# Kernel tuning notes

Hardware: AMD Instinct MI355X
Metric: run time of the kernel (lower is better)

Reference implementation:

```python
import jax, jax.numpy as jnp
import numpy as np

N = 12000   # num_node
D = 128     # hiddenSize
HID = 256   # hidden_channels
B = 512     # batch
L = 20      # citing history length
F = 400     # title_vec + journal_vec
FF = 512    # transformer dim_feedforward
NH = 4      # heads
STDV = float(1.0 / np.sqrt(D))


def _unif(k, shape):
    return jax.random.uniform(k, shape, jnp.float32, -STDV, STDV)


def setup_inputs():
    key = jax.random.key(0)
    ks = jax.random.split(key, 40)
    inp = {}
    inp['embedding'] = _unif(ks[0], (N, D))
    inp['f1_w'] = _unif(ks[1], (D, F)); inp['f1_b'] = _unif(ks[2], (D,))
    # two GNN modules, each a 2-layer GCN (assumed structure)
    inp['gcn0_w1'] = _unif(ks[3], (D, HID)); inp['gcn0_b1'] = _unif(ks[4], (HID,))
    inp['gcn0_w2'] = _unif(ks[5], (HID, D)); inp['gcn0_b2'] = _unif(ks[6], (D,))
    inp['gcn1_w1'] = _unif(ks[7], (D, HID)); inp['gcn1_b1'] = _unif(ks[8], (HID,))
    inp['gcn1_w2'] = _unif(ks[9], (HID, D)); inp['gcn1_b2'] = _unif(ks[10], (D,))
    # transformer encoder layer (post-norm, relu), reset_parameters makes ALL weights uniform
    inp['in_proj_w'] = _unif(ks[11], (3 * D, D)); inp['in_proj_b'] = _unif(ks[12], (3 * D,))
    inp['out_proj_w'] = _unif(ks[13], (D, D)); inp['out_proj_b'] = _unif(ks[14], (D,))
    inp['ln1_s'] = _unif(ks[15], (D,)); inp['ln1_b'] = _unif(ks[16], (D,))
    inp['ff1_w'] = _unif(ks[17], (FF, D)); inp['ff1_b'] = _unif(ks[18], (FF,))
    inp['ff2_w'] = _unif(ks[19], (D, FF)); inp['ff2_b'] = _unif(ks[20], (D,))
    inp['ln2_s'] = _unif(ks[21], (D,)); inp['ln2_b'] = _unif(ks[22], (D,))
    # forward inputs
    inp['adj_mat'] = jax.random.uniform(ks[23], (N, N), jnp.float32) * (2.0 / N)  # ~row-stochastic
    inp['node_feature'] = jax.random.normal(ks[24], (N, F), jnp.float32)
    inp['H_content'] = jax.random.normal(ks[25], (B, 10), jnp.float32)  # unused in forward
    inp['citing'] = jax.random.randint(ks[26], (B,), 0, N)
    inp['h_items'] = jax.random.randint(ks[27], (B,), 0, N)  # unused in forward
    inp['u_seqs'] = jax.random.randint(ks[28], (B, L), 0, N)
    inp['u_seqs_num'] = jax.random.randint(ks[29], (B,), 1, L)  # unused in forward
    return inp


def _layer_norm(x, s, b):
    m = x.mean(-1, keepdims=True)
    v = ((x - m) ** 2).mean(-1, keepdims=True)
    return (x - m) * jax.lax.rsqrt(v + 1e-5) * s + b


def reference(embedding, f1_w, f1_b,
              gcn0_w1, gcn0_b1, gcn0_w2, gcn0_b2,
              gcn1_w1, gcn1_b1, gcn1_w2, gcn1_b2,
              in_proj_w, in_proj_b, out_proj_w, out_proj_b,
              ln1_s, ln1_b, ff1_w, ff1_b, ff2_w, ff2_b, ln2_s, ln2_b,
              adj_mat, node_feature, H_content,
              citing, h_items, u_seqs, u_seqs_num):
    # embedding gate
    nf = node_feature @ f1_w.T + f1_b          # [N, D]
    x = embedding * nf                          # [N, D]
    # GCN stack: each GNN = relu((A x) W1 + b1) -> (A h) W2 + b2
    for (w1, b1, w2, b2) in ((gcn0_w1, gcn0_b1, gcn0_w2, gcn0_b2),
                             (gcn1_w1, gcn1_b1, gcn1_w2, gcn1_b2)):
        h = jax.nn.relu((adj_mat @ x) @ w1 + b1)
        x = (adj_mat @ h) @ w2 + b2
    item = x                                    # [N, D]
    seq = item[u_seqs]                          # [B, L, D]
    # torch TransformerEncoderLayer with batch_first=False: dim0 (B) is the
    # sequence axis, dim1 (L) is the batch axis (faithful to original code).
    qkv = seq @ in_proj_w.T + in_proj_b         # [B, L, 3D]
    q, k, v = jnp.split(qkv, 3, axis=-1)
    dh = D // NH
    q = q.reshape(B, L, NH, dh) * (1.0 / np.sqrt(dh))
    k = k.reshape(B, L, NH, dh)
    v = v.reshape(B, L, NH, dh)
    att = jax.nn.softmax(jnp.einsum('snhd,tnhd->nhst', q, k), axis=-1)  # attn over seq axis s,t=B
    o = jnp.einsum('nhst,tnhd->snhd', att, v).reshape(B, L, D)
    o = o @ out_proj_w.T + out_proj_b
    x1 = _layer_norm(seq + o, ln1_s, ln1_b)
    ff = jax.nn.relu(x1 @ ff1_w.T + ff1_b) @ ff2_w.T + ff2_b
    x2 = _layer_norm(x1 + ff, ln2_s, ln2_b)
    citing_vec = x2.mean(axis=1)                # mean over dim=1 (L), [B, D]
    citing_feats = nf[citing]                   # [B, D]
    citing_paper = jnp.concatenate([citing_vec, citing_feats], axis=1)  # [B, 2D]
    cited_paper = jnp.concatenate([item, nf], axis=1)                   # [N, 2D]
    scores = citing_paper @ cited_paper.T       # [B, N]
    return scores
```

## Files before the change

kernel.cpp:

```cpp
#include <hip/hip_runtime.h>
#include <hip/hip_bf16.h>

typedef __hip_bfloat16 bf;
typedef __attribute__((ext_vector_type(4))) float f32x4;
typedef __attribute__((ext_vector_type(8))) __bf16 bf16x8;
typedef __attribute__((ext_vector_type(8))) short short8;
typedef __attribute__((ext_vector_type(4))) short short4v;

#define NN 12000
#define DD 128
#define HIDC 256
#define BBATCH 512
#define LSEQ 20
#define FFEAT 400
#define FFDIM 512
#define AZ 5
#define AKS (NN / AZ)

__device__ __forceinline__ float b2f(bf v) { return __bfloat162float(v); }
__device__ __forceinline__ bf f2b(float v) { return __float2bfloat16(v); }
__device__ __forceinline__ float us2f(unsigned short u) {
    return __uint_as_float(((unsigned int)u) << 16);
}
__device__ __forceinline__ unsigned short f2us(float f) {
    bf h = __float2bfloat16(f);
    return __builtin_bit_cast(unsigned short, h);
}

__device__ __forceinline__ void gload_lds16(const bf* g, bf* l) {
    __builtin_amdgcn_global_load_lds(
        (__attribute__((address_space(1))) void*)(g),
        (__attribute__((address_space(3))) void*)(l),
        16, 0, 0);
}

template<bool F32>
__device__ __forceinline__ short8 ld8(const void* p, long long idx) {
    if (F32) {
        const float* fp = (const float*)p + idx;
        f32x4 u0 = *(const f32x4*)fp;
        f32x4 u1 = *(const f32x4*)(fp + 4);
        short8 s;
        s[0] = (short)f2us(u0[0]); s[1] = (short)f2us(u0[1]);
        s[2] = (short)f2us(u0[2]); s[3] = (short)f2us(u0[3]);
        s[4] = (short)f2us(u1[0]); s[5] = (short)f2us(u1[1]);
        s[6] = (short)f2us(u1[2]); s[7] = (short)f2us(u1[3]);
        return s;
    } else {
        return *(const short8*)((const bf*)p + idx);
    }
}

template<bool F32>
__device__ __forceinline__ bf ldelem(const void* p, long long idx) {
    if (F32) return f2b(((const float*)p)[idx]);
    return ((const bf*)p)[idx];
}

__global__ __launch_bounds__(512) void adj_gemm8(
    const bf* __restrict__ A,
    const bf* __restrict__ Bt,
    float* __restrict__ part)
{
    alignas(16) __shared__ bf As[4][128 * 64];
    alignas(16) __shared__ bf Bs[4][128 * 64];
    const int tid = threadIdx.x;
    const int lane = tid & 63;
    const int w = tid >> 6;
    const int z = blockIdx.y;
    const long long k0 = (long long)z * AKS;
    int m0 = blockIdx.x * 128;
    if (m0 > NN - 128) m0 = NN - 128;

    const int rowi = lane >> 3;
    const int chks = (lane & 7) ^ rowi;
    const bf* gA[2]; const bf* gB[2]; int lo[2];
    #pragma unroll
    for (int i = 0; i < 2; i++) {
        int rbase = 16 * w + 8 * i;
        gA[i] = A  + (long long)(m0 + rbase + rowi) * NN + k0 + chks * 8;
        gB[i] = Bt + (long long)(rbase + rowi) * NN + k0 + chks * 8;
        lo[i] = rbase * 64;
    }
    const int rowiT = lane >> 2;
    const int chksT = (lane & 3) ^ ((lane >> 3) & 3);
    const bf* gAT = A  + (long long)(m0 + 16 * w + rowiT) * NN + k0 + 2368 + chksT * 8;
    const bf* gBT = Bt + (long long)(16 * w + rowiT) * NN + k0 + 2368 + chksT * 8;
    const int loT = (16 * w) * 32;

    const int wr = (w >> 1) * 32, wc = (w & 1) * 64;
    const int fr = lane & 15;
    const int kq = lane >> 4;
    int aoff[2][2], boff[2][4], aoffT[2], boffT[4];
    #pragma unroll
    for (int mi = 0; mi < 2; mi++) {
        int ra = wr + mi * 16 + fr;
        aoff[0][mi] = ra * 64 + ((kq)     ^ (ra & 7)) * 8;
        aoff[1][mi] = ra * 64 + ((4 + kq) ^ (ra & 7)) * 8;
        aoffT[mi]   = ra * 32 + (kq ^ ((ra >> 1) & 3)) * 8;
    }
    #pragma unroll
    for (int ni = 0; ni < 4; ni++) {
        int rb = wc + ni * 16 + fr;
        boff[0][ni] = rb * 64 + ((kq)     ^ (rb & 7)) * 8;
        boff[1][ni] = rb * 64 + ((4 + kq) ^ (rb & 7)) * 8;
        boffT[ni]   = rb * 32 + (kq ^ ((rb >> 1) & 3)) * 8;
    }
    f32x4 acc[2][4] = {};

    auto stage64 = [&](int t, int b) {
        const long long go = (long long)t * 64;
        const int bo = b * (128 * 64);
        #pragma unroll
        for (int i = 0; i < 2; i++) {
            gload_lds16(gA[i] + go, &As[0][0] + bo + lo[i]);
            gload_lds16(gB[i] + go, &Bs[0][0] + bo + lo[i]);
        }
    };
    auto stageTail = [&]() {
        gload_lds16(gAT, &As[1][0] + loT);
        gload_lds16(gBT, &Bs[1][0] + loT);
    };
    auto compute64 = [&](int b) {
        const bf* Ab = &As[0][0] + b * (128 * 64);
        const bf* Bb = &Bs[0][0] + b * (128 * 64);
        #pragma unroll
        for (int s = 0; s < 2; s++) {
            bf16x8 af[2], bfr[4];
            #pragma unroll
            for (int mi = 0; mi < 2; mi++) af[mi]  = *(const bf16x8*)(Ab + aoff[s][mi]);
            #pragma unroll
            for (int ni = 0; ni < 4; ni++) bfr[ni] = *(const bf16x8*)(Bb + boff[s][ni]);
            #pragma unroll
            for (int mi = 0; mi < 2; mi++)
                #pragma unroll
                for (int ni = 0; ni < 4; ni++)
                    acc[mi][ni] = __builtin_amdgcn_mfma_f32_16x16x32_bf16(
                        af[mi], bfr[ni], acc[mi][ni], 0, 0, 0);
        }
    };

    stage64(0, 0);
    stage64(1, 1);
    stage64(2, 2);

    #pragma unroll 1
    for (int t = 0; t < 35; t++) {
        asm volatile("s_waitcnt vmcnt(8)" ::: "memory");
        __builtin_amdgcn_s_barrier();
        __builtin_amdgcn_sched_barrier(0);
        compute64(t & 3);
        if (t < 34) stage64(t + 3, (t + 3) & 3);
        else        stageTail();
    }
    asm volatile("s_waitcnt vmcnt(6)" ::: "memory");
    __builtin_amdgcn_s_barrier();
    __builtin_amdgcn_sched_barrier(0);
    compute64(3);
    asm volatile("s_waitcnt vmcnt(2)" ::: "memory");
    __builtin_amdgcn_s_barrier();
    __builtin_amdgcn_sched_barrier(0);
    compute64(0);
    asm volatile("s_waitcnt vmcnt(0)" ::: "memory");
    __builtin_amdgcn_s_barrier();
    __builtin_amdgcn_sched_barrier(0);
    {
        bf16x8 af[2], bfr[4];
        #pragma unroll
        for (int mi = 0; mi < 2; mi++) af[mi]  = *(const bf16x8*)(&As[1][0] + aoffT[mi]);
        #pragma unroll
        for (int ni = 0; ni < 4; ni++) bfr[ni] = *(const bf16x8*)(&Bs[1][0] + boffT[ni]);
        #pragma unroll
        for (int mi = 0; mi < 2; mi++)
            #pragma unroll
            for (int ni = 0; ni < 4; ni++)
                acc[mi][ni] = __builtin_amdgcn_mfma_f32_16x16x32_bf16(
                    af[mi], bfr[ni], acc[mi][ni], 0, 0, 0);
    }

    float* C = part + (long long)z * ((long long)NN * 128);
    const int cr0 = (lane >> 4) * 4;
    const int cc = lane & 15;
    #pragma unroll
    for (int mi = 0; mi < 2; mi++) {
        #pragma unroll
        for (int ni = 0; ni < 4; ni++) {
            int col = wc + ni * 16 + cc;
            #pragma unroll
            for (int j = 0; j < 4; j++) {
                int row = m0 + wr + mi * 16 + cr0 + j;
                C[(long long)row * 128 + col] = acc[mi][ni][j];
            }
        }
    }
}

template<bool A_F32, bool B_F32, bool HAS_BIAS, bool RELU, bool OUT_F32, bool SIDE_A>
__global__ __launch_bounds__(256) void gemm128(
    const void* __restrict__ A, int lda, long long sA1, long long sA2,
    const void* __restrict__ Bm, int ldb, long long sB1, long long sB2,
    const float* __restrict__ bias,
    void* __restrict__ Cv, int ldc, long long sC1, long long sC2,
    int M, int N, int K, int tilesN, int zdiv, float alpha,
    bf* __restrict__ sideA)
{
    __shared__ bf As[128][40];
    __shared__ bf Bs[128][40];
    const int tid = threadIdx.x;
    const int z = blockIdx.y;
    const int zq = z / zdiv, zr = z - zq * zdiv;
    const char* Ap = (const char*)A;
    const char* Bp = (const char*)Bm;
    const long long offA = (long long)zq * sA1 + (long long)zr * sA2;
    const long long offB = (long long)zq * sB1 + (long long)zr * sB2;
    const long long offC = (long long)zq * sC1 + (long long)zr * sC2;
    const int tm = blockIdx.x / tilesN, tn = blockIdx.x - tm * tilesN;
    int m0 = tm * 128; if (m0 > M - 128) m0 = M - 128;
    const int n0 = tn * 128;
    const int lane = tid & 63;
    const int wv = tid >> 6;
    const int wr = (wv >> 1) * 64, wc = (wv & 1) * 64;
    const int fr = lane & 15;
    const int kq = (lane >> 4) * 8;
    const int sr = tid >> 2, scol = (tid & 3) * 8;
    f32x4 acc[4][4] = {};

    for (int k0 = 0; k0 < K; k0 += 32) {
        if (k0 + 32 <= K) {
            const long long ia0 = offA + (long long)(m0 + sr) * lda + k0 + scol;
            const long long ia1 = offA + (long long)(m0 + sr + 64) * lda + k0 + scol;
            short8 va0 = ld8<A_F32>(Ap, ia0);
            short8 va1 = ld8<A_F32>(Ap, ia1);
            short8 vb0 = {0,0,0,0,0,0,0,0}, vb1 = {0,0,0,0,0,0,0,0};
            if (n0 + sr < N)      vb0 = ld8<B_F32>(Bp, offB + (long long)(n0 + sr) * ldb + k0 + scol);
            if (n0 + sr + 64 < N) vb1 = ld8<B_F32>(Bp, offB + (long long)(n0 + sr + 64) * ldb + k0 + scol);
            if (SIDE_A) {
                *(short8*)&sideA[ia0] = va0;
                *(short8*)&sideA[ia1] = va1;
            }
            *(short8*)&As[sr][scol] = va0;
            *(short8*)&As[sr + 64][scol] = va1;
            *(short8*)&Bs[sr][scol] = vb0;
            *(short8*)&Bs[sr + 64][scol] = vb1;
        } else {
            bf zv = f2b(0.f);
            for (int i = tid; i < 128 * 32; i += 256) {
                int r = i >> 5, c = i & 31, gk = k0 + c;
                As[r][c] = (gk < K) ? ldelem<A_F32>(Ap, offA + (long long)(m0 + r) * lda + gk) : zv;
                Bs[r][c] = (gk < K && n0 + r < N) ? ldelem<B_F32>(Bp, offB + (long long)(n0 + r) * ldb + gk) : zv;
            }
        }
        __syncthreads();
        bf16x8 af[4], bfg[4];
        #pragma unroll
        for (int i = 0; i < 4; i++) af[i]  = *(const bf16x8*)&As[wr + i * 16 + fr][kq];
        #pragma unroll
        for (int i = 0; i < 4; i++) bfg[i] = *(const bf16x8*)&Bs[wc + i * 16 + fr][kq];
        #pragma unroll
        for (int mi = 0; mi < 4; mi++)
            #pragma unroll
            for (int ni = 0; ni < 4; ni++)
                acc[mi][ni] = __builtin_amdgcn_mfma_f32_16x16x32_bf16(
                    af[mi], bfg[ni], acc[mi][ni], 0, 0, 0);
        __syncthreads();
    }

    const int cr0 = (lane >> 4) * 4;
    const int cc = lane & 15;
    #pragma unroll
    for (int mi = 0; mi < 4; mi++) {
        #pragma unroll
        for (int ni = 0; ni < 4; ni++) {
            int col = n0 + wc + ni * 16 + cc;
            if (col >= N) continue;
            float bv = 0.f;
            if (HAS_BIAS) bv = bias[col];
            #pragma unroll
            for (int j = 0; j < 4; j++) {
                int row = m0 + wr + mi * 16 + cr0 + j;
                float v = acc[mi][ni][j] * alpha + bv;
                if (RELU) v = fmaxf(v, 0.f);
                if (OUT_F32) ((float*)Cv)[offC + (long long)row * ldc + col] = v;
                else ((bf*)Cv)[offC + (long long)row * ldc + col] = f2b(v);
            }
        }
    }
}

__global__ __launch_bounds__(256) void gemm_t2(
    const bf* __restrict__ A,
    const bf* __restrict__ Bw,
    bf* __restrict__ BT)
{
    __shared__ bf As[128][40];
    __shared__ bf Bs[128][40];
    const int tid = threadIdx.x;
    int m0 = blockIdx.x * 128;
    if (m0 > NN - 128) m0 = NN - 128;
    const int lane = tid & 63;
    const int wv = tid >> 6;
    const int wr = (wv >> 1) * 64, wc = (wv & 1) * 64;
    const int fr = lane & 15;
    const int kq = (lane >> 4) * 8;
    const int sr = tid >> 2, scol = (tid & 3) * 8;
    f32x4 acc[4][4] = {};

    for (int k0 = 0; k0 < 256; k0 += 32) {
        *(short8*)&As[sr][scol]      = ld8<false>(A, (long long)(m0 + sr) * 256 + k0 + scol);
        *(short8*)&As[sr + 64][scol] = ld8<false>(A, (long long)(m0 + sr + 64) * 256 + k0 + scol);
        *(short8*)&Bs[sr][scol]      = ld8<false>(Bw, (long long)sr * 256 + k0 + scol);
        *(short8*)&Bs[sr + 64][scol] = ld8<false>(Bw, (long long)(sr + 64) * 256 + k0 + scol);
        __syncthreads();
        bf16x8 af[4], bfg[4];
        #pragma unroll
        for (int i = 0; i < 4; i++) af[i]  = *(const bf16x8*)&As[wr + i * 16 + fr][kq];
        #pragma unroll
        for (int i = 0; i < 4; i++) bfg[i] = *(const bf16x8*)&Bs[wc + i * 16 + fr][kq];
        #pragma unroll
        for (int mi = 0; mi < 4; mi++)
            #pragma unroll
            for (int ni = 0; ni < 4; ni++)
                acc[mi][ni] = __builtin_amdgcn_mfma_f32_16x16x32_bf16(
                    af[mi], bfg[ni], acc[mi][ni], 0, 0, 0);
        __syncthreads();
    }

    const int cr0 = (lane >> 4) * 4;
    const int cc = lane & 15;
    #pragma unroll
    for (int mi = 0; mi < 4; mi++) {
        #pragma unroll
        for (int ni = 0; ni < 4; ni++) {
            int col = wc + ni * 16 + cc;
            int rowb = m0 + wr + mi * 16 + cr0;
            short4v v;
            #pragma unroll
            for (int j = 0; j < 4; j++) v[j] = (short)f2us(acc[mi][ni][j]);
            *(short4v*)&BT[(long long)col * NN + rowb] = v;
        }
    }
}

__global__ __launch_bounds__(256) void reduceKT(
    const float* __restrict__ part, const float* __restrict__ bias,
    bf* __restrict__ BT)
{
    __shared__ bf t[32][33];
    const long long zs = (long long)NN * 128;
    int r0 = blockIdx.x * 32, c0 = blockIdx.y * 32;
    int tx = threadIdx.x, ty = threadIdx.y;
    #pragma unroll
    for (int i = 0; i < 4; i++) {
        int r = r0 + ty + i * 8, c = c0 + tx;
        float s = bias[c];
        #pragma unroll
        for (int z = 0; z < AZ; z++) s += part[(long long)z * zs + (long long)r * 128 + c];
        t[ty + i * 8][tx] = f2b(s);
    }
    __syncthreads();
    #pragma unroll
    for (int i = 0; i < 4; i++) {
        int c = c0 + ty + i * 8, r = r0 + tx;
        BT[(long long)c * NN + r] = t[tx][ty + i * 8];
    }
}

__global__ __launch_bounds__(256) void gemm_ln(
    const bf* __restrict__ A, int lda,
    const float* __restrict__ Bw,
    const float* __restrict__ bias,
    const bf* __restrict__ resid,
    const float* __restrict__ lnS, const float* __restrict__ lnB,
    bf* __restrict__ outp, int K)
{
    __shared__ bf As[128][40];
    __shared__ bf Bs[128][40];
    __shared__ float red[128][2][2];
    const int tid = threadIdx.x;
    const int m0 = blockIdx.x * 128;
    const int lane = tid & 63;
    const int wv = tid >> 6;
    const int wr = (wv >> 1) * 64, wc = (wv & 1) * 64;
    const int fr = lane & 15;
    const int kq = (lane >> 4) * 8;
    const int sr = tid >> 2, scol = (tid & 3) * 8;
    f32x4 acc[4][4] = {};

    for (int k0 = 0; k0 < K; k0 += 32) {
        short8 va0 = ld8<false>(A, (long long)(m0 + sr) * lda + k0 + scol);
        short8 va1 = ld8<false>(A, (long long)(m0 + sr + 64) * lda + k0 + scol);
        short8 vb0 = ld8<true>(Bw, (long long)sr * K + k0 + scol);
        short8 vb1 = ld8<true>(Bw, (long long)(sr + 64) * K + k0 + scol);
        *(short8*)&As[sr][scol] = va0;
        *(short8*)&As[sr + 64][scol] = va1;
        *(short8*)&Bs[sr][scol] = vb0;
        *(short8*)&Bs[sr + 64][scol] = vb1;
        __syncthreads();
        bf16x8 af[4], bfg[4];
        #pragma unroll
        for (int i = 0; i < 4; i++) af[i]  = *(const bf16x8*)&As[wr + i * 16 + fr][kq];
        #pragma unroll
        for (int i = 0; i < 4; i++) bfg[i] = *(const bf16x8*)&Bs[wc + i * 16 + fr][kq];
        #pragma unroll
        for (int mi = 0; mi < 4; mi++)
            #pragma unroll
            for (int ni = 0; ni < 4; ni++)
                acc[mi][ni] = __builtin_amdgcn_mfma_f32_16x16x32_bf16(
                    af[mi], bfg[ni], acc[mi][ni], 0, 0, 0);
        __syncthreads();
    }

    const int cr0 = (lane >> 4) * 4;
    const int cc = lane & 15;
    #pragma unroll
    for (int mi = 0; mi < 4; mi++)
        #pragma unroll
        for (int ni = 0; ni < 4; ni++) {
            int col = wc + ni * 16 + cc;
            #pragma unroll
            for (int j = 0; j < 4; j++) {
                int row = m0 + wr + mi * 16 + cr0 + j;
                acc[mi][ni][j] += bias[col] + b2f(resid[(long long)row * 128 + col]);
            }
        }
    float s1[4][4], s2[4][4];
    #pragma unroll
    for (int mi = 0; mi < 4; mi++)
        #pragma unroll
        for (int j = 0; j < 4; j++) {
            float a = 0.f, b = 0.f;
            #pragma unroll
            for (int ni = 0; ni < 4; ni++) {
                float x = acc[mi][ni][j];
                a += x; b += x * x;
            }
            #pragma unroll
            for (int off = 1; off < 16; off <<= 1) {
                a += __shfl_xor(a, off, 64);
                b += __shfl_xor(b, off, 64);
            }
            s1[mi][j] = a; s2[mi][j] = b;
        }
    if (cc == 0) {
        #pragma unroll
        for (int mi = 0; mi < 4; mi++)
            #pragma unroll
            for (int j = 0; j < 4; j++) {
                int lr = wr + mi * 16 + cr0 + j;
                red[lr][wv & 1][0] = s1[mi][j];
                red[lr][wv & 1][1] = s2[mi][j];
            }
    }
    __syncthreads();
    #pragma unroll
    for (int mi = 0; mi < 4; mi++)
        #pragma unroll
        for (int ni = 0; ni < 4; ni++) {
            int col = wc + ni * 16 + cc;
            float ls = lnS[col], lb = lnB[col];
            #pragma unroll
            for (int j = 0; j < 4; j++) {
                int lr = wr + mi * 16 + cr0 + j;
                float tot  = red[lr][0][0] + red[lr][1][0];
                float tot2 = red[lr][0][1] + red[lr][1][1];
                float mean = tot * (1.f / 128.f);
                float var  = tot2 * (1.f / 128.f) - mean * mean;
                float inv  = rsqrtf(var + 1e-5f);
                outp[(long long)(m0 + lr) * 128 + col] =
                    f2b((acc[mi][ni][j] - mean) * inv * ls + lb);
            }
        }
}

__global__ __launch_bounds__(256) void gemm_scores(
    const bf* __restrict__ A,
    const bf* __restrict__ B1,
    const bf* __restrict__ B2,
    float* __restrict__ outp)
{
    __shared__ bf As[128][40];
    __shared__ bf Bs[128][40];
    const int tid = threadIdx.x;
    const int tm = blockIdx.x / 94, tn = blockIdx.x - tm * 94;
    const int m0 = tm * 128;
    const int n0 = tn * 128;
    const int lane = tid & 63;
    const int wv = tid >> 6;
    const int wr = (wv >> 1) * 64, wc = (wv & 1) * 64;
    const int fr = lane & 15;
    const int kq = (lane >> 4) * 8;
    const int sr = tid >> 2, scol = (tid & 3) * 8;
    f32x4 acc[4][4] = {};

    for (int k0 = 0; k0 < 256; k0 += 32) {
        short8 va0 = ld8<false>(A, (long long)(m0 + sr) * 256 + k0 + scol);
        short8 va1 = ld8<false>(A, (long long)(m0 + sr + 64) * 256 + k0 + scol);
        const int gk = k0 + scol;
        const bf* bb = (gk < 128) ? B1 : B2;
        const int kk = gk & 127;
        short8 vb0 = {0,0,0,0,0,0,0,0}, vb1 = {0,0,0,0,0,0,0,0};
        if (n0 + sr < NN)      vb0 = *(const short8*)(bb + (long long)(n0 + sr) * 128 + kk);
        if (n0 + sr + 64 < NN) vb1 = *(const short8*)(bb + (long long)(n0 + sr + 64) * 128 + kk);
        *(short8*)&As[sr][scol] = va0;
        *(short8*)&As[sr + 64][scol] = va1;
        *(short8*)&Bs[sr][scol] = vb0;
        *(short8*)&Bs[sr + 64][scol] = vb1;
        __syncthreads();
        bf16x8 af[4], bfg[4];
        #pragma unroll
        for (int i = 0; i < 4; i++) af[i]  = *(const bf16x8*)&As[wr + i * 16 + fr][kq];
        #pragma unroll
        for (int i = 0; i < 4; i++) bfg[i] = *(const bf16x8*)&Bs[wc + i * 16 + fr][kq];
        #pragma unroll
        for (int mi = 0; mi < 4; mi++)
            #pragma unroll
            for (int ni = 0; ni < 4; ni++)
                acc[mi][ni] = __builtin_amdgcn_mfma_f32_16x16x32_bf16(
                    af[mi], bfg[ni], acc[mi][ni], 0, 0, 0);
        __syncthreads();
    }

    const int cr0 = (lane >> 4) * 4;
    const int cc = lane & 15;
    #pragma unroll
    for (int mi = 0; mi < 4; mi++) {
        #pragma unroll
        for (int ni = 0; ni < 4; ni++) {
            int col = n0 + wc + ni * 16 + cc;
            if (col >= NN) continue;
            #pragma unroll
            for (int j = 0; j < 4; j++) {
                int row = m0 + wr + mi * 16 + cr0 + j;
                outp[(long long)row * NN + col] = acc[mi][ni][j];
            }
        }
    }
}

__global__ __launch_bounds__(256) void transpose4_k(
    const float* s0, const float* s1, const float* s2, const float* s3,
    bf* d0, bf* d1, bf* d2, bf* d3)
{
    __shared__ bf t[32][33];
    const int z = blockIdx.z;
    const float* in = (z == 0) ? s0 : (z == 1) ? s1 : (z == 2) ? s2 : s3;
    bf* out = (z == 0) ? d0 : (z == 1) ? d1 : (z == 2) ? d2 : d3;
    const int R = (z & 1) ? HIDC : DD;
    const int C = (z & 1) ? DD : HIDC;
    int r0 = blockIdx.x * 32, c0 = blockIdx.y * 32;
    if (r0 >= R || c0 >= C) return;
    int tx = threadIdx.x, ty = threadIdx.y;
    #pragma unroll
    for (int i = 0; i < 4; i++) {
        int r = r0 + ty + i * 8, c = c0 + tx;
        bf v = f2b(0.f);
        if (r < R && c < C) v = f2b(in[(long long)r * C + c]);
        t[ty + i * 8][tx] = v;
    }
    __syncthreads();
    #pragma unroll
    for (int i = 0; i < 4; i++) {
        int c = c0 + ty + i * 8, r = r0 + tx;
        if (c < C && r < R) out[(long long)c * R + r] = t[tx][ty + i * 8];
    }
}

template<bool IN_F32>
__global__ __launch_bounds__(256) void transpose_k(
    const void* __restrict__ in, int ldin, long long sI1, long long sI2, int zdiv,
    const float* __restrict__ mulp, int ldmul,
    bf* __restrict__ outp, int ldout, long long sOut,
    int R, int C)
{
    __shared__ bf t[32][33];
    const int z = blockIdx.z;
    const int zq = z / zdiv, zr = z - zq * zdiv;
    const long long offI = (long long)zq * sI1 + (long long)zr * sI2;
    bf* op = outp + (long long)z * sOut;
    int r0 = blockIdx.x * 32, c0 = blockIdx.y * 32;
    int tx = threadIdx.x, ty = threadIdx.y;
    #pragma unroll
    for (int i = 0; i < 4; i++) {
        int r = r0 + ty + i * 8, c = c0 + tx;
        bf v = f2b(0.f);
        if (r < R && c < C) {
            v = ldelem<IN_F32>(in, offI + (long long)r * ldin + c);
            if (mulp) v = f2b(b2f(v) * mulp[(long long)r * ldmul + c]);
        }
        t[ty + i * 8][tx] = v;
    }
    __syncthreads();
    #pragma unroll
    for (int i = 0; i < 4; i++) {
        int c = c0 + ty + i * 8, r = r0 + tx;
        if (c < C && r < R) op[(long long)c * ldout + r] = t[tx][ty + i * 8];
    }
}

__global__ __launch_bounds__(256) void reduceK(
    const float* __restrict__ part, const float* __restrict__ bias,
    bf* __restrict__ outp, int total, int nz, long long zs)
{
    int i = blockIdx.x * 256 + threadIdx.x;
    if (i >= total) return;
    float s = 0.f;
    for (int zz = 0; zz < nz; zz++) s += part[(long long)zz * zs + i];
    if (bias) s += bias[i & 127];
    outp[i] = f2b(s);
}

__global__ __launch_bounds__(256) void gather_rows(
    const bf* __restrict__ src, const int* __restrict__ idx,
    bf* __restrict__ dst, int nrows)
{
    int t = blockIdx.x * 256 + threadIdx.x;
    int row = t >> 4, p = t & 15;
    if (row >= nrows) return;
    long long srow = idx[row];
    *(short8*)&dst[(long long)row * 128 + p * 8] =
        *(const short8*)&src[srow * 128 + p * 8];
}

__global__ __launch_bounds__(256) void softmax512(bf* __restrict__ S, int nrows)
{
    int gid = blockIdx.x * 256 + threadIdx.x;
    int wid = gid >> 6, lane = gid & 63;
    if (wid >= nrows) return;
    bf* row = S + (long long)wid * 512;
    short8 raw = *(const short8*)&row[lane * 8];
    float v[8];
    float mx = -3.0e38f;
    #pragma unroll
    for (int j = 0; j < 8; j++) {
        v[j] = us2f((unsigned short)raw[j]);
        mx = fmaxf(mx, v[j]);
    }
    #pragma unroll
    for (int off = 32; off; off >>= 1) mx = fmaxf(mx, __shfl_xor(mx, off, 64));
    float sum = 0.f;
    #pragma unroll
    for (int j = 0; j < 8; j++) { v[j] = __expf(v[j] - mx); sum += v[j]; }
    #pragma unroll
    for (int off = 32; off; off >>= 1) sum += __shfl_xor(sum, off, 64);
    float inv = 1.f / sum;
    short8 o;
    #pragma unroll
    for (int j = 0; j < 8; j++) o[j] = (short)f2us(v[j] * inv);
    *(short8*)&row[lane * 8] = o;
}

__global__ __launch_bounds__(256) void build_citing(
    const bf* __restrict__ x2, const bf* __restrict__ nf,
    const int* __restrict__ citing, bf* __restrict__ cp)
{
    int i = blockIdx.x * 256 + threadIdx.x;
    if (i >= BBATCH * 256) return;
    int b = i >> 8, d = i & 255;
    float v;
    if (d < 128) {
        float s = 0.f;
        for (int l = 0; l < LSEQ; l++)
            s += b2f(x2[((long long)b * LSEQ + l) * 128 + d]);
        v = s * (1.f / (float)LSEQ);
    } else {
        v = b2f(nf[(long long)citing[b] * 128 + (d - 128)]);
    }
    cp[i] = f2b(v);
}

extern "C" void kernel_launch(void* const* d_in, const int* in_sizes, int n_in,
                              void* d_out, int out_size, void* d_ws, size_t ws_size,
                              hipStream_t stream)
{
    const float* emb  = (const float*)d_in[0];
    const float* f1w  = (const float*)d_in[1];
    const float* f1b  = (const float*)d_in[2];
    const float* g0w1 = (const float*)d_in[3];  const float* g0b1 = (const float*)d_in[4];
    const float* g0w2 = (const float*)d_in[5];  const float* g0b2 = (const float*)d_in[6];
    const float* g1w1 = (const float*)d_in[7];  const float* g1b1 = (const float*)d_in[8];
    const float* g1w2 = (const float*)d_in[9];  const float* g1b2 = (const float*)d_in[10];
    const float* ipw  = (const float*)d_in[11]; const float* ipb  = (const float*)d_in[12];
    const float* opw  = (const float*)d_in[13]; const float* opb  = (const float*)d_in[14];
    const float* ln1s = (const float*)d_in[15]; const float* ln1b = (const float*)d_in[16];
    const float* ff1w = (const float*)d_in[17]; const float* ff1b = (const float*)d_in[18];
    const float* ff2w = (const float*)d_in[19]; const float* ff2b = (const float*)d_in[20];
    const float* ln2s = (const float*)d_in[21]; const float* ln2b = (const float*)d_in[22];
    const float* adj  = (const float*)d_in[23];
    const float* nfe  = (const float*)d_in[24];
    const int* citing = (const int*)d_in[26];
    const int* useqs  = (const int*)d_in[28];
    float* outp = (float*)d_out;

    size_t off = 0;
    auto carve = [&](size_t bytes) -> char* {
        char* p = (char*)d_ws + off;
        off += (bytes + 255) & ~(size_t)255;
        return p;
    };
    bf* adjb = (bf*)carve((size_t)NN * NN * 2);
    bf* nf   = (bf*)carve((size_t)NN * DD * 2);
    bf* bufP = (bf*)carve((size_t)NN * DD * 2);
    bf* bufQ = (bf*)carve((size_t)NN * DD * 2);
    bf* BT   = (bf*)carve((size_t)NN * DD * 2);
    bf* Hbuf = (bf*)carve((size_t)NN * HIDC * 2);
    float* part = (float*)carve((size_t)AZ * NN * DD * 4);
    bf* seq  = (bf*)carve((size_t)10240 * DD * 2);
    bf* qkv  = (bf*)carve((size_t)10240 * 384 * 2);
    bf* Sb   = (bf*)carve((size_t)80 * 512 * 512 * 2);
    bf* w10T = (bf*)carve((size_t)DD * HIDC * 2);
    bf* w20T = (bf*)carve((size_t)DD * HIDC * 2);
    bf* w11T = (bf*)carve((size_t)DD * HIDC * 2);
    bf* w21T = (bf*)carve((size_t)DD * HIDC * 2);
    bf* x1ln = (bf*)Hbuf;
    bf* cp   = (bf*)((char*)Hbuf + (size_t)10240 * DD * 2);
    char* pr = (char*)part;
    bf* VT   = (bf*)pr; pr += (size_t)80 * 32 * 512 * 2;
    bf* o_   = (bf*)pr; pr += (size_t)10240 * DD * 2;
    bf* ffh  = (bf*)pr; pr += (size_t)10240 * FFDIM * 2;
    bf* x2   = (bf*)pr; pr += (size_t)10240 * DD * 2;

    dim3 tb(256), tb512(512), tt(32, 8);
    const long long NM = (long long)NN * DD;

    transpose4_k<<<dim3(8, 8, 4), tt, 0, stream>>>(
        g0w1, g0w2, g1w1, g1w2, w10T, w20T, w11T, w21T);

    gemm128<true, true, true, false, false, false><<<dim3(94, 1), tb, 0, stream>>>(
        nfe, FFEAT, 0, 0, f1w, FFEAT, 0, 0, f1b,
        nf, DD, 0, 0, NN, DD, FFEAT, 1, 1, 1.f, nullptr);
    transpose_k<false><<<dim3(375, 4, 1), tt, 0, stream>>>(nf, DD, 0, 0, 1, emb, DD, BT, NN, 0, NN, DD);

    const float* biases1[2] = { g0b1, g1b1 };
    const bf* w1T[2] = { w10T, w11T };
    const bf* w2T[2] = { w20T, w21T };

    for (int g = 0; g < 2; g++) {
        if (g == 0) {
            gemm128<true, false, false, false, true, true><<<dim3(94, AZ), tb, 0, stream>>>(
                adj, NN, AKS, 0, BT, NN, AKS, 0, nullptr,
                part, DD, NM, 0, NN, DD, AKS, 1, 1, 1.f, adjb);
        } else {
            adj_gemm8<<<dim3(94, AZ), tb512, 0, stream>>>(adjb, BT, part);
        }
        bf* tbuf = (g == 0) ? bufP : bufQ;
        reduceK<<<dim3((NM + 255) / 256), tb, 0, stream>>>(part, nullptr, tbuf, (int)NM, AZ, NM);
        gemm128<false, false, true, true, false, false><<<dim3(188, 1), tb, 0, stream>>>(
            tbuf, DD, 0, 0, w1T[g], DD, 0, 0, biases1[g],
            Hbuf, HIDC, 0, 0, NN, HIDC, DD, 2, 1, 1.f, nullptr);
        gemm_t2<<<dim3(94), tb, 0, stream>>>(Hbuf, w2T[g], BT);
        adj_gemm8<<<dim3(94, AZ), tb512, 0, stream>>>(adjb, BT, part);
        if (g == 0) {
            reduceKT<<<dim3(375, 4), tt, 0, stream>>>(part, g0b2, BT);
        } else {
            reduceK<<<dim3((NM + 255) / 256), tb, 0, stream>>>(part, g1b2, bufQ, (int)NM, AZ, NM);
        }
    }
    bf* item = bufQ;

    gather_rows<<<dim3(640), tb, 0, stream>>>(item, useqs, seq, 10240);
    gemm128<false, true, true, false, false, false><<<dim3(240, 1), tb, 0, stream>>>(
        seq, DD, 0, 0, ipw, DD, 0, 0, ipb,
        qkv, 384, 0, 0, 10240, 384, DD, 3, 1, 1.f, nullptr);
    transpose_k<false><<<dim3(16, 1, 80), tt, 0, stream>>>(
        qkv + 256, 7680, 384, 32, 4, nullptr, 0, VT, 512, 16384, 512, 32);
    gemm128<false, false, false, false, false, false><<<dim3(16, 80), tb, 0, stream>>>(
        qkv, 7680, 384, 32, qkv + 128, 7680, 384, 32, nullptr,
        Sb, 512, (long long)4 * 262144, 262144, 512, 512, 32, 4, 4, 0.17677669529663687f, nullptr);
    softmax512<<<dim3(10240), tb, 0, stream>>>(Sb, 80 * 512);
    gemm128<false, false, false, false, false, false><<<dim3(4, 80), tb, 0, stream>>>(
        Sb, 512, (long long)4 * 262144, 262144, VT, 512, (long long)4 * 16384, 16384, nullptr,
        o_, 2560, 128, 32, 512, 32, 512, 1, 4, 1.f, nullptr);
    gemm_ln<<<dim3(80), tb, 0, stream>>>(o_, DD, opw, opb, seq, ln1s, ln1b, x1ln, DD);
    gemm128<false, true, true, true, false, false><<<dim3(320, 1), tb, 0, stream>>>(
        x1ln, DD, 0, 0, ff1w, DD, 0, 0, ff1b,
        ffh, FFDIM, 0, 0, 10240, FFDIM, DD, 4, 1, 1.f, nullptr);
    gemm_ln<<<dim3(80), tb, 0, stream>>>(ffh, FFDIM, ff2w, ff2b, x1ln, ln2s, ln2b, x2, FFDIM);
    build_citing<<<dim3(512), tb, 0, stream>>>(x2, nf, citing, cp);
    gemm_scores<<<dim3(376), tb, 0, stream>>>(cp, item, nf, outp);
}
```

Before: 726.3 us.

## Fuse attention QK^T, softmax and PV into one kernel

```diff
diff --git a/kernel.cpp b/kernel.cpp
--- a/kernel.cpp
+++ b/kernel.cpp
@@ -287,6 +287,115 @@
     }
 }
 
+__global__ __launch_bounds__(256) void attn_fused(
+    const bf* __restrict__ qkv,
+    const bf* __restrict__ VTg,
+    bf* __restrict__ o_)
+{
+    __shared__ bf Qs[64][40];
+    __shared__ bf Ks[512][40];
+    __shared__ bf Ps[64][136];
+    const int tid = threadIdx.x;
+    const int lane = tid & 63;
+    const int w = tid >> 6;
+    const int z = blockIdx.y;
+    const int n = z >> 2, h = z & 3;
+    const int m0 = blockIdx.x * 64;
+    const int qbase = n * 384 + h * 32;
+    const int kbase = qbase + 128;
+
+    {
+        int row = tid >> 2, part = tid & 3;
+        *(short8*)&Qs[row][part * 8] =
+            *(const short8*)(qkv + (long long)(m0 + row) * 7680 + qbase + part * 8);
+    }
+    #pragma unroll
+    for (int i = 0; i < 8; i++) {
+        int idx = i * 256 + tid;
+        int row = idx >> 2, part = idx & 3;
+        *(short8*)&Ks[row][part * 8] =
+            *(const short8*)(qkv + (long long)row * 7680 + kbase + part * 8);
+    }
+    __syncthreads();
+
+    const int fr = lane & 15;
+    const int kq8 = (lane >> 4) * 8;
+    const bf16x8 aq = *(const bf16x8*)&Qs[16 * w + fr][kq8];
+    f32x4 acc[32];
+    #pragma unroll
+    for (int ni = 0; ni < 32; ni++) {
+        bf16x8 bk = *(const bf16x8*)&Ks[ni * 16 + fr][kq8];
+        acc[ni] = __builtin_amdgcn_mfma_f32_16x16x32_bf16(
+            aq, bk, f32x4{0.f, 0.f, 0.f, 0.f}, 0, 0, 0);
+    }
+
+    const float alpha = 0.17677669529663687f;
+    float mx[4] = {-3e38f, -3e38f, -3e38f, -3e38f};
+    #pragma unroll
+    for (int ni = 0; ni < 32; ni++)
+        #pragma unroll
+        for (int j = 0; j < 4; j++) mx[j] = fmaxf(mx[j], acc[ni][j]);
+    #pragma unroll
+    for (int j = 0; j < 4; j++) {
+        #pragma unroll
+        for (int off = 1; off < 16; off <<= 1)
+            mx[j] = fmaxf(mx[j], __shfl_xor(mx[j], off, 64));
+        mx[j] *= alpha;
+    }
+    float sum[4] = {0.f, 0.f, 0.f, 0.f};
+    #pragma unroll
+    for (int ni = 0; ni < 32; ni++)
+        #pragma unroll
+        for (int j = 0; j < 4; j++) {
+            float p = __expf(acc[ni][j] * alpha - mx[j]);
+            acc[ni][j] = p;
+            sum[j] += p;
+        }
+    #pragma unroll
+    for (int j = 0; j < 4; j++) {
+        #pragma unroll
+        for (int off = 1; off < 16; off <<= 1)
+            sum[j] += __shfl_xor(sum[j], off, 64);
+        sum[j] = 1.f / sum[j];
+    }
+
+    const int prow = 16 * w + (lane >> 4) * 4;
+    f32x4 oacc[2] = {};
+    const bf* vtz = VTg + (long long)z * 16384;
+    #pragma unroll 1
+    for (int c = 0; c < 4; c++) {
+        #pragma unroll
+        for (int t8 = 0; t8 < 8; t8++) {
+            int ni = c * 8 + t8;
+            #pragma unroll
+            for (int j = 0; j < 4; j++)
+                Ps[prow + j][t8 * 16 + fr] = f2b(acc[ni][j]);
+        }
+        __syncthreads();
+        #pragma unroll
+        for (int kc = 0; kc < 4; kc++) {
+            bf16x8 pa = *(const bf16x8*)&Ps[16 * w + fr][kc * 32 + kq8];
+            #pragma unroll
+            for (int nj = 0; nj < 2; nj++) {
+                bf16x8 bv = *(const bf16x8*)(vtz + (long long)(nj * 16 + fr) * 512
+                                              + c * 128 + kc * 32 + kq8);
+                oacc[nj] = __builtin_amdgcn_mfma_f32_16x16x32_bf16(
+                    pa, bv, oacc[nj], 0, 0, 0);
+            }
+        }
+        __syncthreads();
+    }
+
+    #pragma unroll
+    for (int nj = 0; nj < 2; nj++)
+        #pragma unroll
+        for (int j = 0; j < 4; j++) {
+            int s = m0 + prow + j;
+            int d = nj * 16 + fr;
+            o_[(long long)s * 2560 + n * 128 + h * 32 + d] = f2b(oacc[nj][j] * sum[j]);
+        }
+}
+
 __global__ __launch_bounds__(256) void gemm_t2(
     const bf* __restrict__ A,
     const bf* __restrict__ Bw,
@@ -619,34 +728,6 @@
     long long srow = idx[row];
     *(short8*)&dst[(long long)row * 128 + p * 8] =
         *(const short8*)&src[srow * 128 + p * 8];
-}
-
-__global__ __launch_bounds__(256) void softmax512(bf* __restrict__ S, int nrows)
-{
-    int gid = blockIdx.x * 256 + threadIdx.x;
-    int wid = gid >> 6, lane = gid & 63;
-    if (wid >= nrows) return;
-    bf* row = S + (long long)wid * 512;
-    short8 raw = *(const short8*)&row[lane * 8];
-    float v[8];
-    float mx = -3.0e38f;
-    #pragma unroll
-    for (int j = 0; j < 8; j++) {
-        v[j] = us2f((unsigned short)raw[j]);
-        mx = fmaxf(mx, v[j]);
-    }
-    #pragma unroll
-    for (int off = 32; off; off >>= 1) mx = fmaxf(mx, __shfl_xor(mx, off, 64));
-    float sum = 0.f;
-    #pragma unroll
-    for (int j = 0; j < 8; j++) { v[j] = __expf(v[j] - mx); sum += v[j]; }
-    #pragma unroll
-    for (int off = 32; off; off >>= 1) sum += __shfl_xor(sum, off, 64);
-    float inv = 1.f / sum;
-    short8 o;
-    #pragma unroll
-    for (int j = 0; j < 8; j++) o[j] = (short)f2us(v[j] * inv);
-    *(short8*)&row[lane * 8] = o;
 }
 
 __global__ __launch_bounds__(256) void build_citing(
@@ -706,7 +787,6 @@
     float* part = (float*)carve((size_t)AZ * NN * DD * 4);
     bf* seq  = (bf*)carve((size_t)10240 * DD * 2);
     bf* qkv  = (bf*)carve((size_t)10240 * 384 * 2);
-    bf* Sb   = (bf*)carve((size_t)80 * 512 * 512 * 2);
     bf* w10T = (bf*)carve((size_t)DD * HIDC * 2);
     bf* w20T = (bf*)carve((size_t)DD * HIDC * 2);
     bf* w11T = (bf*)carve((size_t)DD * HIDC * 2);
@@ -763,13 +843,7 @@
         qkv, 384, 0, 0, 10240, 384, DD, 3, 1, 1.f, nullptr);
     transpose_k<false><<<dim3(16, 1, 80), tt, 0, stream>>>(
         qkv + 256, 7680, 384, 32, 4, nullptr, 0, VT, 512, 16384, 512, 32);
-    gemm128<false, false, false, false, false, false><<<dim3(16, 80), tb, 0, stream>>>(
-        qkv, 7680, 384, 32, qkv + 128, 7680, 384, 32, nullptr,
-        Sb, 512, (long long)4 * 262144, 262144, 512, 512, 32, 4, 4, 0.17677669529663687f, nullptr);
-    softmax512<<<dim3(10240), tb, 0, stream>>>(Sb, 80 * 512);
-    gemm128<false, false, false, false, false, false><<<dim3(4, 80), tb, 0, stream>>>(
-        Sb, 512, (long long)4 * 262144, 262144, VT, 512, (long long)4 * 16384, 16384, nullptr,
-        o_, 2560, 128, 32, 512, 32, 512, 1, 4, 1.f, nullptr);
+    attn_fused<<<dim3(8, 80), tb, 0, stream>>>(qkv, VT, o_);
     gemm_ln<<<dim3(80), tb, 0, stream>>>(o_, DD, opw, opb, seq, ln1s, ln1b, x1ln, DD);
     gemm128<false, true, true, true, false, false><<<dim3(320, 1), tb, 0, stream>>>(
         x1ln, DD, 0, 0, ff1w, DD, 0, 0, ff1b,
```

Measured after the change: 735.9 us. Within noise of the previous version (+1.3%).
